# Kernel optimization log

Hardware: AMD Instinct MI355X
Metric: run time of the kernel (lower is better)

The kernel has to match this reference:

```python
import jax, jax.numpy as jnp
import numpy as np

N_SEG = 128      # number of ragged segments (boundaries has N_SEG+1 entries)
SEG_LEN = 128    # tokens per segment (regular boundaries)
D_IN = 1024      # input_size
H = 512          # hidden per direction; output_size = 2*H = 1024


def _run_dir(xs, W_ih, W_hh, b):
    """xs: [L, B, D] -> hidden states [L, B, H] for one direction.
    torch LSTM gate order: i, f, g, o."""
    xp = jnp.einsum('lbd,gd->lbg', xs, W_ih) + b  # precompute input projections [L,B,4H]
    B = xs.shape[1]
    Hh = W_hh.shape[1]

    def step(carry, gx):
        h, c = carry
        g = gx + h @ W_hh.T
        i, f, gg, o = jnp.split(g, 4, axis=-1)
        c = jax.nn.sigmoid(f) * c + jax.nn.sigmoid(i) * jnp.tanh(gg)
        h = jax.nn.sigmoid(o) * jnp.tanh(c)
        return (h, c), h

    z = jnp.zeros((B, Hh), xs.dtype)
    _, hs = jax.lax.scan(step, (z, z), xp)
    return hs


def _bilstm(x, W_ih_f, W_hh_f, b_f, W_ih_b, W_hh_b, b_b):
    hf = _run_dir(x, W_ih_f, W_hh_f, b_f)
    hb = _run_dir(x[::-1], W_ih_b, W_hh_b, b_b)[::-1]
    return jnp.concatenate([hf, hb], axis=-1)  # [L, B, 2H], fwd then bwd as in torch


def setup_inputs() -> dict:
    key = jax.random.key(0)
    ks = jax.random.split(key, 7)
    T = N_SEG * SEG_LEN
    s = 1.0 / np.sqrt(H)  # torch LSTM init scale
    u = lambda k, shape: jax.random.uniform(k, shape, jnp.float32, -s, s)
    return {
        'all_embs': jax.random.normal(ks[0], (T, D_IN), jnp.float32),
        'boundaries': jnp.arange(N_SEG + 1, dtype=jnp.int32) * SEG_LEN,
        'W_ih_f': u(ks[1], (4 * H, D_IN)),
        'W_hh_f': u(ks[2], (4 * H, H)),
        'b_f': u(ks[3], (4 * H,)),  # b_ih + b_hh folded together
        'W_ih_b': u(ks[4], (4 * H, D_IN)),
        'W_hh_b': u(ks[5], (4 * H, H)),
        'b_b': u(ks[6], (4 * H,)),
    }


def reference(all_embs, boundaries, W_ih_f, W_hh_f, b_f, W_ih_b, W_hh_b, b_b):
    n_seg = boundaries.shape[0] - 1
    T, D = all_embs.shape
    L = T // n_seg
    # regular boundaries: batch the per-segment LSTM calls into one scan
    x = all_embs.reshape(n_seg, L, D).transpose(1, 0, 2)  # [L, n_seg, D]
    y = _bilstm(x, W_ih_f, W_hh_f, b_f, W_ih_b, W_hh_b, b_b)  # [L, n_seg, 2H]
    out = y.transpose(1, 0, 2).reshape(T, 2 * H)
    # summarize=False: new boundaries equal old boundaries
    return (out, boundaries)
```

## Files before the change

### kernel.cpp

```cpp
#include <hip/hip_runtime.h>


typedef __attribute__((ext_vector_type(8))) short bf16x8;
typedef __attribute__((ext_vector_type(4))) float f32x4;

__device__ __forceinline__ unsigned short f2bf(float f) {
  unsigned int x = __builtin_bit_cast(unsigned int, f);
  x += 0x7fffu + ((x >> 16) & 1u);
  return (unsigned short)(x >> 16);
}
__device__ __forceinline__ float bf2f(unsigned short u) {
  unsigned int x = ((unsigned int)u) << 16;
  return __builtin_bit_cast(float, x);
}
__device__ __forceinline__ float sigm(float x) { return 1.f / (1.f + __expf(-x)); }
__device__ __forceinline__ float tanhfast(float x) {
  float e = __expf(2.f * x);
  return 1.f - 2.f / (e + 1.f);
}

__device__ __forceinline__ void gl_lds16(const void* g, void* l) {
  __builtin_amdgcn_global_load_lds((const __attribute__((address_space(1))) unsigned int*)g,
                                   (__attribute__((address_space(3))) unsigned int*)l, 16, 0, 0);
}
__device__ __forceinline__ void gl_lds16_llc(const void* g, void* l) {
  __builtin_amdgcn_global_load_lds((const __attribute__((address_space(1))) unsigned int*)g,
                                   (__attribute__((address_space(3))) unsigned int*)l, 16, 0, 17);
}

__global__ __launch_bounds__(256) void cast_x(const float* __restrict__ X,
                                              unsigned short* __restrict__ Xb) {
  const int i = blockIdx.x * 256 + threadIdx.x;
  const float4 v = ((const float4*)X)[i];
  uint2 o;
  o.x = (unsigned int)f2bf(v.x) | ((unsigned int)f2bf(v.y) << 16);
  o.y = (unsigned int)f2bf(v.z) | ((unsigned int)f2bf(v.w) << 16);
  ((uint2*)Xb)[i] = o;
}

__global__ __launch_bounds__(256) void pack_w(const float* __restrict__ Wif,
                                              const float* __restrict__ bf_,
                                              const float* __restrict__ Wib,
                                              const float* __restrict__ bb_,
                                              unsigned short* __restrict__ Wc,
                                              float* __restrict__ biasp) {
  const int pr = blockIdx.x;
  const int d = pr >> 11, r = pr & 2047;
  const float* src = (d ? Wib : Wif) + (size_t)r * 1024;
  const int t = threadIdx.x;
  const float4 v = ((const float4*)src)[t];
  uint2 o;
  o.x = (unsigned int)f2bf(v.x) | ((unsigned int)f2bf(v.y) << 16);
  o.y = (unsigned int)f2bf(v.z) | ((unsigned int)f2bf(v.w) << 16);
  ((uint2*)(Wc + (size_t)pr * 1024))[t] = o;
  if (t == 0) biasp[pr] = (d ? bb_ : bf_)[r];
}

__global__ __launch_bounds__(512) void gemm_xp(const unsigned short* __restrict__ A,
                                               const unsigned short* __restrict__ B,
                                               const float* __restrict__ bias,
                                               unsigned short* __restrict__ C) {
  __shared__ unsigned short SMEM[65536];
  const int tid = threadIdx.x;
  const int lane = tid & 63;
  const int wid = tid >> 6;
  const int wm = wid >> 2;
  const int wn = wid & 3;
  const int nid = blockIdx.x;
  const int xcd = nid & 7;
  const int ii = nid >> 3;
  const int bx = ii & 63;
  const int by = xcd * 2 + (ii >> 6);
  const long brow = (long)bx * 256;
  const long bcol = (long)by * 256;

  f32x4 acc[8][4];
  const f32x4 z = {0.f, 0.f, 0.f, 0.f};
#pragma unroll
  for (int m = 0; m < 8; ++m)
#pragma unroll
    for (int n = 0; n < 4; ++n) acc[m][n] = z;

  int srow[2], scol[2];
#pragma unroll
  for (int j = 0; j < 2; ++j) {
    const int o = (j * 512 + tid) * 16;
    srow[j] = o >> 7;
    scol[j] = (o & 127) ^ ((srow[j] & 7) << 4);
  }

#define STAGE_HALF(t, h, buf)                                                          \
  do {                                                                                 \
    const char* aA_ = (const char*)A + (brow + (h)*128) * 2048 + (t)*128;              \
    const char* aB_ = (const char*)B + (bcol + (h)*128) * 2048 + (t)*128;              \
    char* dA_ = (char*)(SMEM + ((buf)*2 + (h)) * 8192);                                \
    char* dB_ = (char*)(SMEM + 32768 + ((buf)*2 + (h)) * 8192);                        \
    _Pragma("unroll") for (int j_ = 0; j_ < 2; ++j_) {                                 \
      const int o_ = (j_ * 512 + tid) * 16;                                            \
      gl_lds16(aA_ + (long)srow[j_] * 2048 + scol[j_], dA_ + o_);                      \
      gl_lds16(aB_ + (long)srow[j_] * 2048 + scol[j_], dB_ + o_);                      \
    }                                                                                  \
  } while (0)

  STAGE_HALF(0, 0, 0);
  STAGE_HALF(0, 1, 0);

  const int p15 = lane & 15;
  const int kq = lane >> 4;

  for (int t = 0; t < 16; ++t) {
    const int cur = t & 1, nxt = cur ^ 1;
    const bool doStage = (t + 1 < 16);
    const unsigned short* Acur = SMEM + (cur * 2 + wm) * 8192;
    const unsigned short* Bcur = SMEM + 32768 + (cur * 2 + (wn >> 1)) * 8192;
#pragma unroll
    for (int p = 0; p < 4; ++p) {
      if (p < 2 && doStage) STAGE_HALF(t + 1, p, nxt);
      if (p == 0) {
        if (doStage)
          asm volatile("s_waitcnt vmcnt(4)" ::: "memory");
        else
          asm volatile("s_waitcnt vmcnt(0)" ::: "memory");
      }
      __builtin_amdgcn_s_barrier();
      bf16x8 af[2][2], bf[4][2];
#pragma unroll
      for (int mm = 0; mm < 2; ++mm) {
        const int ar = (2 * p + mm) * 16 + p15;
        const char* abase = (const char*)Acur + ar * 128;
        const int asw = (ar & 7) << 4;
#pragma unroll
        for (int kk = 0; kk < 2; ++kk)
          af[mm][kk] = *(const bf16x8*)(abase + ((kk * 64 + kq * 16) ^ asw));
      }
#pragma unroll
      for (int n = 0; n < 4; ++n) {
        const int br = (wn & 1) * 64 + n * 16 + p15;
        const char* bbase = (const char*)Bcur + br * 128;
        const int bsw = (br & 7) << 4;
#pragma unroll
        for (int kk = 0; kk < 2; ++kk)
          bf[n][kk] = *(const bf16x8*)(bbase + ((kk * 64 + kq * 16) ^ bsw));
      }
      __builtin_amdgcn_s_setprio(1);
#pragma unroll
      for (int kk = 0; kk < 2; ++kk)
#pragma unroll
        for (int mm = 0; mm < 2; ++mm)
#pragma unroll
          for (int n = 0; n < 4; ++n)
            acc[2 * p + mm][n] = __builtin_amdgcn_mfma_f32_16x16x32_bf16(
                af[mm][kk], bf[n][kk], acc[2 * p + mm][n], 0, 0, 0);
      __builtin_amdgcn_s_setprio(0);
      __builtin_amdgcn_s_barrier();
    }
  }
#undef STAGE_HALF

  __syncthreads();
  const int crow0 = wm * 128 + kq * 4;
  const int ccol0 = wn * 64 + p15;
#pragma unroll
  for (int m = 0; m < 8; ++m) {
#pragma unroll
    for (int n = 0; n < 4; ++n) {
      const int col = ccol0 + n * 16;
      const float bsv = bias[bcol + col];
#pragma unroll
      for (int r = 0; r < 4; ++r)
        SMEM[(crow0 + m * 16 + r) * 256 + col] = f2bf(acc[m][n][r] + bsv);
    }
  }
  __syncthreads();
#pragma unroll
  for (int i = 0; i < 16; ++i) {
    const int id = i * 512 + tid;
    const int row = id >> 5;
    const int c = id & 31;
    *(float4*)(C + (brow + row) * 4096 + bcol + c * 8) =
        *(const float4*)(SMEM + row * 256 + c * 8);
  }
}

__global__ __launch_bounds__(256, 1) void lstm_persist(
    const unsigned short* __restrict__ XPb, const float* __restrict__ Whf,
    const float* __restrict__ Whb, unsigned short* __restrict__ hb0,
    unsigned short* __restrict__ hb1, float* __restrict__ out,
    unsigned int* __restrict__ ctr) {
  __shared__ unsigned short A_s[8192];
  __shared__ unsigned short Hrep[16][32];

  const int tid = threadIdx.x;
  const int bid = blockIdx.x;
  const int ut = bid >> 4;
  const int grp = bid & 15;
  const int dir = grp >> 3;
  const int cs = grp & 7;
  const int lane = tid & 63;
  const int w = tid >> 6;
  const int p = lane & 15;
  const int kq8 = lane >> 4;
  const int hi = p >> 3;
  const int u_l = w * 8 + (p & 7);
  const int u_g = ut * 32 + u_l;
  unsigned int* const myctr = ctr + grp * 32;

  bf16x8 wreg[2][16];
  {
    const float* Wh = dir ? Whb : Whf;
#pragma unroll
    for (int f = 0; f < 2; ++f) {
      const int g = f * 2 + hi;
      const float* wrow = Wh + (size_t)(g * 512 + u_g) * 512 + kq8 * 8;
#pragma unroll
      for (int kk = 0; kk < 16; ++kk) {
        const float4 v0 = *(const float4*)(wrow + kk * 32);
        const float4 v1 = *(const float4*)(wrow + kk * 32 + 4);
        bf16x8 t;
        t[0] = (short)f2bf(v0.x); t[1] = (short)f2bf(v0.y);
        t[2] = (short)f2bf(v0.z); t[3] = (short)f2bf(v0.w);
        t[4] = (short)f2bf(v1.x); t[5] = (short)f2bf(v1.y);
        t[6] = (short)f2bf(v1.z); t[7] = (short)f2bf(v1.w);
        wreg[f][kk] = t;
      }
    }
  }

  float c_reg[2] = {0.f, 0.f};
  const size_t tileoff = (size_t)grp * 16384;
  const int cl0 = kq8 * 4 + 2 * hi;

  unsigned short xpr[2][4];
  {
    const int tcol0 = dir ? 127 : 0;
#pragma unroll
    for (int j = 0; j < 2; ++j) {
      const int seg = cs * 16 + cl0 + j;
      const size_t tok = (size_t)seg * 128 + tcol0;
      const unsigned short* xp = XPb + tok * 4096 + dir * 2048 + u_g;
#pragma unroll
      for (int g = 0; g < 4; ++g) xpr[j][g] = xp[g * 512];
    }
  }

  float phv[2];
  size_t pofs[2] = {0, 0};

  for (int tau = 0; tau < 128; ++tau) {
    const unsigned short* hc = (tau & 1) ? hb1 : hb0;
    unsigned short* hn = (tau & 1) ? hb0 : hb1;
    const int tcol = dir ? (127 - tau) : tau;

    {
      const char* srcb = (const char*)hc + tileoff;
      char* dstb = (char*)A_s;
#pragma unroll
      for (int j = 0; j < 4; ++j) {
        const int o = (j * 256 + tid) * 16;
        gl_lds16_llc(srcb + o, dstb + o);
      }
    }
    if (tau > 0) {
      out[pofs[0]] = phv[0];
      out[pofs[1]] = phv[1];
    }
    __syncthreads();

    unsigned short xprN[2][4];
    if (tau < 127) {
      const int tcolN = dir ? (126 - tau) : (tau + 1);
#pragma unroll
      for (int j = 0; j < 2; ++j) {
        const int seg = cs * 16 + cl0 + j;
        const size_t tok = (size_t)seg * 128 + tcolN;
        const unsigned short* xp = XPb + tok * 4096 + dir * 2048 + u_g;
#pragma unroll
        for (int g = 0; g < 4; ++g) xprN[j][g] = xp[g * 512];
      }
    }

    f32x4 accp[2][2];
    const f32x4 z = {0.f, 0.f, 0.f, 0.f};
    accp[0][0] = z; accp[0][1] = z; accp[1][0] = z; accp[1][1] = z;
    {
      const char* abase = (const char*)A_s + p * 1024;
      const int asw = (p & 7) << 4;
#pragma unroll
      for (int kk = 0; kk < 16; ++kk) {
        const int kb = kk * 64 + kq8 * 16;
        const bf16x8 af = *(const bf16x8*)(abase + (kb ^ asw));
        accp[0][kk & 1] =
            __builtin_amdgcn_mfma_f32_16x16x32_bf16(af, wreg[0][kk], accp[0][kk & 1], 0, 0, 0);
        accp[1][kk & 1] =
            __builtin_amdgcn_mfma_f32_16x16x32_bf16(af, wreg[1][kk], accp[1][kk & 1], 0, 0, 0);
      }
    }
    f32x4 acc0, acc1;
#pragma unroll
    for (int r = 0; r < 4; ++r) {
      acc0[r] = accp[0][0][r] + accp[0][1][r];
      acc1[r] = accp[1][0][r] + accp[1][1][r];
    }

    float hvr[2];
    {
      const float s0 = hi ? acc0[0] : acc0[2];
      const float s1 = hi ? acc0[1] : acc0[3];
      const float s2 = hi ? acc1[0] : acc1[2];
      const float s3 = hi ? acc1[1] : acc1[3];
      const float e0 = __shfl_xor(s0, 8);
      const float e1 = __shfl_xor(s1, 8);
      const float e2 = __shfl_xor(s2, 8);
      const float e3 = __shfl_xor(s3, 8);
      const float a0 = hi ? acc0[2] : acc0[0];
      const float a1 = hi ? acc0[3] : acc0[1];
      const float b0 = hi ? acc1[2] : acc1[0];
      const float b1 = hi ? acc1[3] : acc1[1];
      const float gi[2] = {hi ? e0 : a0, hi ? e1 : a1};
      const float gf[2] = {hi ? a0 : e0, hi ? a1 : e1};
      const float gg[2] = {hi ? e2 : b0, hi ? e3 : b1};
      const float go[2] = {hi ? b0 : e2, hi ? b1 : e3};
#pragma unroll
      for (int j = 0; j < 2; ++j) {
        const int cl = cl0 + j;
        const float pi = gi[j] + bf2f(xpr[j][0]);
        const float pf = gf[j] + bf2f(xpr[j][1]);
        const float pg = gg[j] + bf2f(xpr[j][2]);
        const float po = go[j] + bf2f(xpr[j][3]);
        float cv = sigm(pf) * c_reg[j] + sigm(pi) * tanhfast(pg);
        c_reg[j] = cv;
        hvr[j] = sigm(po) * tanhfast(cv);
        Hrep[cl][u_l] = f2bf(hvr[j]);
        const int seg = cs * 16 + cl;
        const size_t tok = (size_t)seg * 128 + tcol;
        pofs[j] = tok * 1024 + dir * 512 + u_g;
        phv[j] = hvr[j];
      }
    }
#pragma unroll
    for (int j = 0; j < 2; ++j)
#pragma unroll
      for (int g = 0; g < 4; ++g) xpr[j][g] = xprN[j][g];

    __syncthreads();

    if (tid < 128) {
      const int cl = tid >> 3, q = tid & 7;
      const unsigned long long v = *(const unsigned long long*)&Hrep[cl][q * 4];
      char* dst = (char*)hn + tileoff + cl * 1024 + ((ut * 64 + q * 8) ^ ((cl & 7) << 4));
      __hip_atomic_store((unsigned long long*)dst, v, __ATOMIC_RELAXED,
                         __HIP_MEMORY_SCOPE_AGENT);
    }

    __syncthreads();
    if (tid == 0) {
      const unsigned old =
          __hip_atomic_fetch_add(myctr, 1u, __ATOMIC_RELAXED, __HIP_MEMORY_SCOPE_AGENT);
      const unsigned tgt = (unsigned)(tau + 1) * 16u;
      if (old + 1u != tgt) {
        while (__hip_atomic_load(myctr, __ATOMIC_RELAXED, __HIP_MEMORY_SCOPE_AGENT) < tgt)
          __builtin_amdgcn_s_sleep(1);
      }
    }
    __syncthreads();
  }
  out[pofs[0]] = phv[0];
  out[pofs[1]] = phv[1];
}

__global__ void wr_bounds(const int* __restrict__ b, float* __restrict__ o) {
  const int i = threadIdx.x;
  if (i < 129) o[i] = (float)b[i];
}

extern "C" void kernel_launch(void* const* d_in, const int* in_sizes, int n_in,
                              void* d_out, int out_size, void* d_ws, size_t ws_size,
                              hipStream_t stream) {
  const float* X = (const float*)d_in[0];
  const int* bnd = (const int*)d_in[1];
  const float* Wif = (const float*)d_in[2];
  const float* Whf = (const float*)d_in[3];
  const float* bf_ = (const float*)d_in[4];
  const float* Wib = (const float*)d_in[5];
  const float* Whb = (const float*)d_in[6];
  const float* bb_ = (const float*)d_in[7];
  float* out = (float*)d_out;

  wr_bounds<<<1, 256, 0, stream>>>(bnd, out + 16777216);

  char* ws = (char*)d_ws;
  const size_t NEED = 176703488ULL;
  if (ws_size < NEED) return;

  unsigned short* XPb = (unsigned short*)(ws + 0);
  unsigned short* Xb = (unsigned short*)(ws + 134217728);
  unsigned short* Wc = (unsigned short*)(ws + 167772160);
  float* biasp = (float*)(ws + 176160768);
  unsigned short* hb0 = (unsigned short*)(ws + 176177152);
  unsigned short* hb1 = (unsigned short*)(ws + 176439296);
  unsigned int* ctrp = (unsigned int*)(ws + 176701440);

  cast_x<<<16384, 256, 0, stream>>>(X, Xb);
  pack_w<<<4096, 256, 0, stream>>>(Wif, bf_, Wib, bb_, Wc, biasp);
  gemm_xp<<<1024, 512, 0, stream>>>(Xb, Wc, biasp, XPb);

  hipMemsetAsync(hb0, 0, 262144, stream);
  hipMemsetAsync(ctrp, 0, 2048, stream);

  {
    const unsigned short* xpb = XPb;
    const float* whf = Whf;
    const float* whb = Whb;
    unsigned short* h0 = hb0;
    unsigned short* h1 = hb1;
    float* op = out;
    unsigned int* cp = ctrp;
    void* args[] = {&xpb, &whf, &whb, &h0, &h1, &op, &cp};
    hipError_t e = hipLaunchCooperativeKernel((const void*)lstm_persist, dim3(256), dim3(256),
                                              args, 0, stream);
    if (e != hipSuccess) {
      lstm_persist<<<256, 256, 0, stream>>>(XPb, Whf, Whb, hb0, hb1, out, ctrp);
    }
  }
}
```

Before: 491.8 us.

## Fuse input-projection GEMM with persistent BiLSTM via per-timestep readiness flags

Merges the input-projection GEMM and the persistent recurrent kernel into one cooperative launch. 128 blocks compute GEMM tiles in time-step order, alternating from both ends so forward and backward directions get their inputs early, and publish per-timestep-pair flags. The other 128 blocks run the recurrence with 512 threads (64 hidden units each, half as many blocks per sync group) and spin on those flags before loading each step's projections. The XP layout becomes time-major so each GEMM tile covers whole timesteps. The aim is to overlap the large GEMM with the latency-bound recurrence, at the cost of halving the recurrence block count, which adds per-step work and may slow the critical path while GEMM blocks compete for bandwidth.

```diff
diff --git a/kernel.cpp b/kernel.cpp
--- a/kernel.cpp
+++ b/kernel.cpp
@@ -56,316 +56,338 @@
   if (t == 0) biasp[pr] = (d ? bb_ : bf_)[r];
 }
 
-__global__ __launch_bounds__(512) void gemm_xp(const unsigned short* __restrict__ A,
-                                               const unsigned short* __restrict__ B,
-                                               const float* __restrict__ bias,
-                                               unsigned short* __restrict__ C) {
+__global__ __launch_bounds__(512, 1) void fused_bilstm(
+    const unsigned short* __restrict__ A,
+    const unsigned short* __restrict__ B,
+    const float* __restrict__ bias,
+    unsigned short* __restrict__ XPb,
+    const float* __restrict__ Whf, const float* __restrict__ Whb,
+    unsigned short* __restrict__ hb0, unsigned short* __restrict__ hb1,
+    float* __restrict__ out, unsigned int* __restrict__ ctr,
+    unsigned int* __restrict__ flags) {
   __shared__ unsigned short SMEM[65536];
   const int tid = threadIdx.x;
+  const int bidg = blockIdx.x;
   const int lane = tid & 63;
-  const int wid = tid >> 6;
-  const int wm = wid >> 2;
-  const int wn = wid & 3;
-  const int nid = blockIdx.x;
-  const int xcd = nid & 7;
-  const int ii = nid >> 3;
-  const int bx = ii & 63;
-  const int by = xcd * 2 + (ii >> 6);
-  const long brow = (long)bx * 256;
-  const long bcol = (long)by * 256;
-
-  f32x4 acc[8][4];
-  const f32x4 z = {0.f, 0.f, 0.f, 0.f};
-#pragma unroll
-  for (int m = 0; m < 8; ++m)
-#pragma unroll
-    for (int n = 0; n < 4; ++n) acc[m][n] = z;
-
-  int srow[2], scol[2];
-#pragma unroll
-  for (int j = 0; j < 2; ++j) {
-    const int o = (j * 512 + tid) * 16;
-    srow[j] = o >> 7;
-    scol[j] = (o & 127) ^ ((srow[j] & 7) << 4);
-  }
-
-#define STAGE_HALF(t, h, buf)                                                          \
-  do {                                                                                 \
-    const char* aA_ = (const char*)A + (brow + (h)*128) * 2048 + (t)*128;              \
-    const char* aB_ = (const char*)B + (bcol + (h)*128) * 2048 + (t)*128;              \
-    char* dA_ = (char*)(SMEM + ((buf)*2 + (h)) * 8192);                                \
-    char* dB_ = (char*)(SMEM + 32768 + ((buf)*2 + (h)) * 8192);                        \
-    _Pragma("unroll") for (int j_ = 0; j_ < 2; ++j_) {                                 \
-      const int o_ = (j_ * 512 + tid) * 16;                                            \
-      gl_lds16(aA_ + (long)srow[j_] * 2048 + scol[j_], dA_ + o_);                      \
-      gl_lds16(aB_ + (long)srow[j_] * 2048 + scol[j_], dB_ + o_);                      \
-    }                                                                                  \
+
+  if (bidg < 128) {
+    const int pid = bidg;
+    const int wid = tid >> 6;
+    const int wm = wid >> 2;
+    const int wn = wid & 3;
+    const int p15 = lane & 15;
+    const int kq = lane >> 4;
+
+    int srow[2], scol[2];
+#pragma unroll
+    for (int j = 0; j < 2; ++j) {
+      const int o = (j * 512 + tid) * 16;
+      srow[j] = o >> 7;
+      scol[j] = (o & 127) ^ ((srow[j] & 7) << 4);
+    }
+
+    for (int it = 0; it < 8; ++it) {
+      const int L = pid + it * 128;
+      const int k = L >> 4;
+      const int nt = L & 15;
+      const int pm = (k & 1) ? (63 - (k >> 1)) : (k >> 1);
+      const long brow = (long)pm * 256;
+      const long bcol = (long)nt * 256;
+
+      f32x4 acc[8][4];
+      const f32x4 z = {0.f, 0.f, 0.f, 0.f};
+#pragma unroll
+      for (int m = 0; m < 8; ++m)
+#pragma unroll
+        for (int n = 0; n < 4; ++n) acc[m][n] = z;
+
+#define STAGE_HALF(t, h, buf)                                                        \
+  do {                                                                               \
+    char* dA_ = (char*)(SMEM + ((buf)*2 + (h)) * 8192);                              \
+    char* dB_ = (char*)(SMEM + 32768 + ((buf)*2 + (h)) * 8192);                      \
+    _Pragma("unroll") for (int j_ = 0; j_ < 2; ++j_) {                               \
+      const int o_ = (j_ * 512 + tid) * 16;                                          \
+      const int rA_ = (int)brow + (h)*128 + srow[j_];                                \
+      const long tokA_ = ((long)(rA_ & 127) << 7) + (rA_ >> 7);                      \
+      gl_lds16((const char*)A + tokA_ * 2048 + (t)*128 + scol[j_], dA_ + o_);        \
+      const long rB_ = bcol + (h)*128 + srow[j_];                                    \
+      gl_lds16((const char*)B + rB_ * 2048 + (t)*128 + scol[j_], dB_ + o_);          \
+    }                                                                                \
   } while (0)
 
-  STAGE_HALF(0, 0, 0);
-  STAGE_HALF(0, 1, 0);
-
-  const int p15 = lane & 15;
-  const int kq = lane >> 4;
-
-  for (int t = 0; t < 16; ++t) {
-    const int cur = t & 1, nxt = cur ^ 1;
-    const bool doStage = (t + 1 < 16);
-    const unsigned short* Acur = SMEM + (cur * 2 + wm) * 8192;
-    const unsigned short* Bcur = SMEM + 32768 + (cur * 2 + (wn >> 1)) * 8192;
-#pragma unroll
-    for (int p = 0; p < 4; ++p) {
-      if (p < 2 && doStage) STAGE_HALF(t + 1, p, nxt);
-      if (p == 0) {
-        if (doStage)
-          asm volatile("s_waitcnt vmcnt(4)" ::: "memory");
-        else
-          asm volatile("s_waitcnt vmcnt(0)" ::: "memory");
-      }
-      __builtin_amdgcn_s_barrier();
-      bf16x8 af[2][2], bf[4][2];
-#pragma unroll
-      for (int mm = 0; mm < 2; ++mm) {
-        const int ar = (2 * p + mm) * 16 + p15;
-        const char* abase = (const char*)Acur + ar * 128;
-        const int asw = (ar & 7) << 4;
-#pragma unroll
-        for (int kk = 0; kk < 2; ++kk)
-          af[mm][kk] = *(const bf16x8*)(abase + ((kk * 64 + kq * 16) ^ asw));
-      }
-#pragma unroll
-      for (int n = 0; n < 4; ++n) {
-        const int br = (wn & 1) * 64 + n * 16 + p15;
-        const char* bbase = (const char*)Bcur + br * 128;
-        const int bsw = (br & 7) << 4;
-#pragma unroll
-        for (int kk = 0; kk < 2; ++kk)
-          bf[n][kk] = *(const bf16x8*)(bbase + ((kk * 64 + kq * 16) ^ bsw));
-      }
-      __builtin_amdgcn_s_setprio(1);
-#pragma unroll
-      for (int kk = 0; kk < 2; ++kk)
-#pragma unroll
-        for (int mm = 0; mm < 2; ++mm)
-#pragma unroll
-          for (int n = 0; n < 4; ++n)
-            acc[2 * p + mm][n] = __builtin_amdgcn_mfma_f32_16x16x32_bf16(
-                af[mm][kk], bf[n][kk], acc[2 * p + mm][n], 0, 0, 0);
-      __builtin_amdgcn_s_setprio(0);
-      __builtin_amdgcn_s_barrier();
-    }
-  }
+      STAGE_HALF(0, 0, 0);
+      STAGE_HALF(0, 1, 0);
+
+      for (int t = 0; t < 16; ++t) {
+        const int cur = t & 1, nxt = cur ^ 1;
+        const bool doStage = (t + 1 < 16);
+        const unsigned short* Acur = SMEM + (cur * 2 + wm) * 8192;
+        const unsigned short* Bcur = SMEM + 32768 + (cur * 2 + (wn >> 1)) * 8192;
+#pragma unroll
+        for (int p = 0; p < 4; ++p) {
+          if (p < 2 && doStage) STAGE_HALF(t + 1, p, nxt);
+          if (p == 0) {
+            if (doStage)
+              asm volatile("s_waitcnt vmcnt(4)" ::: "memory");
+            else
+              asm volatile("s_waitcnt vmcnt(0)" ::: "memory");
+          }
+          __builtin_amdgcn_s_barrier();
+          bf16x8 af[2][2], bf[4][2];
+#pragma unroll
+          for (int mm = 0; mm < 2; ++mm) {
+            const int ar = (2 * p + mm) * 16 + p15;
+            const char* abase = (const char*)Acur + ar * 128;
+            const int asw = (ar & 7) << 4;
+#pragma unroll
+            for (int kk = 0; kk < 2; ++kk)
+              af[mm][kk] = *(const bf16x8*)(abase + ((kk * 64 + kq * 16) ^ asw));
+          }
+#pragma unroll
+          for (int n = 0; n < 4; ++n) {
+            const int br = (wn & 1) * 64 + n * 16 + p15;
+            const char* bbase = (const char*)Bcur + br * 128;
+            const int bsw = (br & 7) << 4;
+#pragma unroll
+            for (int kk = 0; kk < 2; ++kk)
+              bf[n][kk] = *(const bf16x8*)(bbase + ((kk * 64 + kq * 16) ^ bsw));
+          }
+          __builtin_amdgcn_s_setprio(1);
+#pragma unroll
+          for (int kk = 0; kk < 2; ++kk)
+#pragma unroll
+            for (int mm = 0; mm < 2; ++mm)
+#pragma unroll
+              for (int n = 0; n < 4; ++n)
+                acc[2 * p + mm][n] = __builtin_amdgcn_mfma_f32_16x16x32_bf16(
+                    af[mm][kk], bf[n][kk], acc[2 * p + mm][n], 0, 0, 0);
+          __builtin_amdgcn_s_setprio(0);
+          __builtin_amdgcn_s_barrier();
+        }
+      }
 #undef STAGE_HALF
 
-  __syncthreads();
-  const int crow0 = wm * 128 + kq * 4;
-  const int ccol0 = wn * 64 + p15;
-#pragma unroll
-  for (int m = 0; m < 8; ++m) {
-#pragma unroll
-    for (int n = 0; n < 4; ++n) {
-      const int col = ccol0 + n * 16;
-      const float bsv = bias[bcol + col];
-#pragma unroll
-      for (int r = 0; r < 4; ++r)
-        SMEM[(crow0 + m * 16 + r) * 256 + col] = f2bf(acc[m][n][r] + bsv);
-    }
-  }
-  __syncthreads();
-#pragma unroll
-  for (int i = 0; i < 16; ++i) {
-    const int id = i * 512 + tid;
-    const int row = id >> 5;
-    const int c = id & 31;
-    *(float4*)(C + (brow + row) * 4096 + bcol + c * 8) =
-        *(const float4*)(SMEM + row * 256 + c * 8);
-  }
-}
-
-__global__ __launch_bounds__(256, 1) void lstm_persist(
-    const unsigned short* __restrict__ XPb, const float* __restrict__ Whf,
-    const float* __restrict__ Whb, unsigned short* __restrict__ hb0,
-    unsigned short* __restrict__ hb1, float* __restrict__ out,
-    unsigned int* __restrict__ ctr) {
-  __shared__ unsigned short A_s[8192];
-  __shared__ unsigned short Hrep[16][32];
-
-  const int tid = threadIdx.x;
-  const int bid = blockIdx.x;
-  const int ut = bid >> 4;
-  const int grp = bid & 15;
-  const int dir = grp >> 3;
-  const int cs = grp & 7;
-  const int lane = tid & 63;
-  const int w = tid >> 6;
-  const int p = lane & 15;
-  const int kq8 = lane >> 4;
-  const int hi = p >> 3;
-  const int u_l = w * 8 + (p & 7);
-  const int u_g = ut * 32 + u_l;
-  unsigned int* const myctr = ctr + grp * 32;
-
-  bf16x8 wreg[2][16];
-  {
-    const float* Wh = dir ? Whb : Whf;
-#pragma unroll
-    for (int f = 0; f < 2; ++f) {
-      const int g = f * 2 + hi;
-      const float* wrow = Wh + (size_t)(g * 512 + u_g) * 512 + kq8 * 8;
-#pragma unroll
-      for (int kk = 0; kk < 16; ++kk) {
-        const float4 v0 = *(const float4*)(wrow + kk * 32);
-        const float4 v1 = *(const float4*)(wrow + kk * 32 + 4);
-        bf16x8 t;
-        t[0] = (short)f2bf(v0.x); t[1] = (short)f2bf(v0.y);
-        t[2] = (short)f2bf(v0.z); t[3] = (short)f2bf(v0.w);
-        t[4] = (short)f2bf(v1.x); t[5] = (short)f2bf(v1.y);
-        t[6] = (short)f2bf(v1.z); t[7] = (short)f2bf(v1.w);
-        wreg[f][kk] = t;
-      }
-    }
-  }
-
-  float c_reg[2] = {0.f, 0.f};
-  const size_t tileoff = (size_t)grp * 16384;
-  const int cl0 = kq8 * 4 + 2 * hi;
-
-  unsigned short xpr[2][4];
-  {
-    const int tcol0 = dir ? 127 : 0;
-#pragma unroll
-    for (int j = 0; j < 2; ++j) {
-      const int seg = cs * 16 + cl0 + j;
-      const size_t tok = (size_t)seg * 128 + tcol0;
-      const unsigned short* xp = XPb + tok * 4096 + dir * 2048 + u_g;
-#pragma unroll
-      for (int g = 0; g < 4; ++g) xpr[j][g] = xp[g * 512];
-    }
-  }
-
-  float phv[2];
-  size_t pofs[2] = {0, 0};
-
-  for (int tau = 0; tau < 128; ++tau) {
-    const unsigned short* hc = (tau & 1) ? hb1 : hb0;
-    unsigned short* hn = (tau & 1) ? hb0 : hb1;
-    const int tcol = dir ? (127 - tau) : tau;
-
+      __syncthreads();
+      const int crow0 = wm * 128 + kq * 4;
+      const int ccol0 = wn * 64 + p15;
+#pragma unroll
+      for (int m = 0; m < 8; ++m) {
+#pragma unroll
+        for (int n = 0; n < 4; ++n) {
+          const int col = ccol0 + n * 16;
+          const float bsv = bias[bcol + col];
+#pragma unroll
+          for (int r = 0; r < 4; ++r)
+            SMEM[(crow0 + m * 16 + r) * 256 + col] = f2bf(acc[m][n][r] + bsv);
+        }
+      }
+      __syncthreads();
+#pragma unroll
+      for (int i = 0; i < 16; ++i) {
+        const int id = i * 512 + tid;
+        const int row = id >> 5;
+        const int c = id & 31;
+        *(float4*)(XPb + (brow + row) * 4096 + bcol + c * 8) =
+            *(const float4*)(SMEM + row * 256 + c * 8);
+      }
+      __syncthreads();
+      if (tid == 0) {
+        __hip_atomic_fetch_add(flags + pm * 32, 1u, __ATOMIC_RELEASE,
+                               __HIP_MEMORY_SCOPE_AGENT);
+      }
+      __syncthreads();
+    }
+  } else {
+    unsigned short* A_s = SMEM;
+    unsigned short(*Hrep)[64] = (unsigned short(*)[64])(SMEM + 8192);
+
+    const int cid = bidg - 128;
+    const int ut = cid >> 4;
+    const int grp = cid & 15;
+    const int dir = grp >> 3;
+    const int cs = grp & 7;
+    const int w = tid >> 6;
+    const int p = lane & 15;
+    const int kq8 = lane >> 4;
+    const int hi = p >> 3;
+    const int u_l = w * 8 + (p & 7);
+    const int u_g = ut * 64 + u_l;
+    unsigned int* const myctr = ctr + grp * 32;
+
+    bf16x8 wreg[2][16];
     {
-      const char* srcb = (const char*)hc + tileoff;
-      char* dstb = (char*)A_s;
-#pragma unroll
-      for (int j = 0; j < 4; ++j) {
-        const int o = (j * 256 + tid) * 16;
-        gl_lds16_llc(srcb + o, dstb + o);
-      }
-    }
-    if (tau > 0) {
-      out[pofs[0]] = phv[0];
-      out[pofs[1]] = phv[1];
-    }
-    __syncthreads();
-
-    unsigned short xprN[2][4];
-    if (tau < 127) {
-      const int tcolN = dir ? (126 - tau) : (tau + 1);
+      const float* Wh = dir ? Whb : Whf;
+#pragma unroll
+      for (int f = 0; f < 2; ++f) {
+        const int g = f * 2 + hi;
+        const float* wrow = Wh + (size_t)(g * 512 + u_g) * 512 + kq8 * 8;
+#pragma unroll
+        for (int kk = 0; kk < 16; ++kk) {
+          const float4 v0 = *(const float4*)(wrow + kk * 32);
+          const float4 v1 = *(const float4*)(wrow + kk * 32 + 4);
+          bf16x8 t;
+          t[0] = (short)f2bf(v0.x); t[1] = (short)f2bf(v0.y);
+          t[2] = (short)f2bf(v0.z); t[3] = (short)f2bf(v0.w);
+          t[4] = (short)f2bf(v1.x); t[5] = (short)f2bf(v1.y);
+          t[6] = (short)f2bf(v1.z); t[7] = (short)f2bf(v1.w);
+          wreg[f][kk] = t;
+        }
+      }
+    }
+
+    float c_reg[2] = {0.f, 0.f};
+    const size_t tileoff = (size_t)grp * 16384;
+    const int cl0 = kq8 * 4 + 2 * hi;
+
+    unsigned short xpr[2][4];
+    {
+      const int tcol0 = dir ? 127 : 0;
+      if (tid == 0) {
+        while (__hip_atomic_load(flags + (tcol0 >> 1) * 32, __ATOMIC_RELAXED,
+                                 __HIP_MEMORY_SCOPE_AGENT) < 16u)
+          __builtin_amdgcn_s_sleep(1);
+      }
+      __syncthreads();
 #pragma unroll
       for (int j = 0; j < 2; ++j) {
         const int seg = cs * 16 + cl0 + j;
-        const size_t tok = (size_t)seg * 128 + tcolN;
-        const unsigned short* xp = XPb + tok * 4096 + dir * 2048 + u_g;
-#pragma unroll
-        for (int g = 0; g < 4; ++g) xprN[j][g] = xp[g * 512];
-      }
-    }
-
-    f32x4 accp[2][2];
-    const f32x4 z = {0.f, 0.f, 0.f, 0.f};
-    accp[0][0] = z; accp[0][1] = z; accp[1][0] = z; accp[1][1] = z;
-    {
-      const char* abase = (const char*)A_s + p * 1024;
-      const int asw = (p & 7) << 4;
-#pragma unroll
-      for (int kk = 0; kk < 16; ++kk) {
-        const int kb = kk * 64 + kq8 * 16;
-        const bf16x8 af = *(const bf16x8*)(abase + (kb ^ asw));
-        accp[0][kk & 1] =
-            __builtin_amdgcn_mfma_f32_16x16x32_bf16(af, wreg[0][kk], accp[0][kk & 1], 0, 0, 0);
-        accp[1][kk & 1] =
-            __builtin_amdgcn_mfma_f32_16x16x32_bf16(af, wreg[1][kk], accp[1][kk & 1], 0, 0, 0);
-      }
-    }
-    f32x4 acc0, acc1;
-#pragma unroll
-    for (int r = 0; r < 4; ++r) {
-      acc0[r] = accp[0][0][r] + accp[0][1][r];
-      acc1[r] = accp[1][0][r] + accp[1][1][r];
-    }
-
-    float hvr[2];
-    {
-      const float s0 = hi ? acc0[0] : acc0[2];
-      const float s1 = hi ? acc0[1] : acc0[3];
-      const float s2 = hi ? acc1[0] : acc1[2];
-      const float s3 = hi ? acc1[1] : acc1[3];
-      const float e0 = __shfl_xor(s0, 8);
-      const float e1 = __shfl_xor(s1, 8);
-      const float e2 = __shfl_xor(s2, 8);
-      const float e3 = __shfl_xor(s3, 8);
-      const float a0 = hi ? acc0[2] : acc0[0];
-      const float a1 = hi ? acc0[3] : acc0[1];
-      const float b0 = hi ? acc1[2] : acc1[0];
-      const float b1 = hi ? acc1[3] : acc1[1];
-      const float gi[2] = {hi ? e0 : a0, hi ? e1 : a1};
-      const float gf[2] = {hi ? a0 : e0, hi ? a1 : e1};
-      const float gg[2] = {hi ? e2 : b0, hi ? e3 : b1};
-      const float go[2] = {hi ? b0 : e2, hi ? b1 : e3};
-#pragma unroll
-      for (int j = 0; j < 2; ++j) {
-        const int cl = cl0 + j;
-        const float pi = gi[j] + bf2f(xpr[j][0]);
-        const float pf = gf[j] + bf2f(xpr[j][1]);
-        const float pg = gg[j] + bf2f(xpr[j][2]);
-        const float po = go[j] + bf2f(xpr[j][3]);
-        float cv = sigm(pf) * c_reg[j] + sigm(pi) * tanhfast(pg);
-        c_reg[j] = cv;
-        hvr[j] = sigm(po) * tanhfast(cv);
-        Hrep[cl][u_l] = f2bf(hvr[j]);
-        const int seg = cs * 16 + cl;
-        const size_t tok = (size_t)seg * 128 + tcol;
-        pofs[j] = tok * 1024 + dir * 512 + u_g;
-        phv[j] = hvr[j];
-      }
-    }
-#pragma unroll
-    for (int j = 0; j < 2; ++j)
-#pragma unroll
-      for (int g = 0; g < 4; ++g) xpr[j][g] = xprN[j][g];
-
-    __syncthreads();
-
-    if (tid < 128) {
-      const int cl = tid >> 3, q = tid & 7;
-      const unsigned long long v = *(const unsigned long long*)&Hrep[cl][q * 4];
-      char* dst = (char*)hn + tileoff + cl * 1024 + ((ut * 64 + q * 8) ^ ((cl & 7) << 4));
-      __hip_atomic_store((unsigned long long*)dst, v, __ATOMIC_RELAXED,
-                         __HIP_MEMORY_SCOPE_AGENT);
-    }
-
-    __syncthreads();
-    if (tid == 0) {
-      const unsigned old =
-          __hip_atomic_fetch_add(myctr, 1u, __ATOMIC_RELAXED, __HIP_MEMORY_SCOPE_AGENT);
-      const unsigned tgt = (unsigned)(tau + 1) * 16u;
-      if (old + 1u != tgt) {
-        while (__hip_atomic_load(myctr, __ATOMIC_RELAXED, __HIP_MEMORY_SCOPE_AGENT) < tgt)
+        const size_t tokp = (size_t)tcol0 * 128 + seg;
+        const unsigned short* xp = XPb + tokp * 4096 + dir * 2048 + u_g;
+#pragma unroll
+        for (int g = 0; g < 4; ++g) xpr[j][g] = xp[g * 512];
+      }
+    }
+
+    float phv[2];
+    size_t pofs[2] = {0, 0};
+
+    for (int tau = 0; tau < 128; ++tau) {
+      const unsigned short* hc = (tau & 1) ? hb1 : hb0;
+      unsigned short* hn = (tau & 1) ? hb0 : hb1;
+      const int tcol = dir ? (127 - tau) : tau;
+
+      {
+        const char* srcb = (const char*)hc + tileoff;
+        char* dstb = (char*)A_s;
+#pragma unroll
+        for (int j = 0; j < 2; ++j) {
+          const int o = (j * 512 + tid) * 16;
+          gl_lds16_llc(srcb + o, dstb + o);
+        }
+      }
+      if (tau > 0) {
+        out[pofs[0]] = phv[0];
+        out[pofs[1]] = phv[1];
+      }
+      if (tau < 127 && tid == 0) {
+        const int tcolN = dir ? (126 - tau) : (tau + 1);
+        while (__hip_atomic_load(flags + (tcolN >> 1) * 32, __ATOMIC_RELAXED,
+                                 __HIP_MEMORY_SCOPE_AGENT) < 16u)
           __builtin_amdgcn_s_sleep(1);
       }
-    }
-    __syncthreads();
+      __syncthreads();
+
+      unsigned short xprN[2][4];
+      if (tau < 127) {
+        const int tcolN = dir ? (126 - tau) : (tau + 1);
+#pragma unroll
+        for (int j = 0; j < 2; ++j) {
+          const int seg = cs * 16 + cl0 + j;
+          const size_t tokp = (size_t)tcolN * 128 + seg;
+          const unsigned short* xp = XPb + tokp * 4096 + dir * 2048 + u_g;
+#pragma unroll
+          for (int g = 0; g < 4; ++g) xprN[j][g] = xp[g * 512];
+        }
+      }
+
+      f32x4 accp[2][2];
+      const f32x4 z = {0.f, 0.f, 0.f, 0.f};
+      accp[0][0] = z; accp[0][1] = z; accp[1][0] = z; accp[1][1] = z;
+      {
+        const char* abase = (const char*)A_s + p * 1024;
+        const int asw = (p & 7) << 4;
+#pragma unroll
+        for (int kk = 0; kk < 16; ++kk) {
+          const int kb = kk * 64 + kq8 * 16;
+          const bf16x8 af = *(const bf16x8*)(abase + (kb ^ asw));
+          accp[0][kk & 1] =
+              __builtin_amdgcn_mfma_f32_16x16x32_bf16(af, wreg[0][kk], accp[0][kk & 1], 0, 0, 0);
+          accp[1][kk & 1] =
+              __builtin_amdgcn_mfma_f32_16x16x32_bf16(af, wreg[1][kk], accp[1][kk & 1], 0, 0, 0);
+        }
+      }
+      f32x4 acc0, acc1;
+#pragma unroll
+      for (int r = 0; r < 4; ++r) {
+        acc0[r] = accp[0][0][r] + accp[0][1][r];
+        acc1[r] = accp[1][0][r] + accp[1][1][r];
+      }
+
+      float hvr[2];
+      {
+        const float s0 = hi ? acc0[0] : acc0[2];
+        const float s1 = hi ? acc0[1] : acc0[3];
+        const float s2 = hi ? acc1[0] : acc1[2];
+        const float s3 = hi ? acc1[1] : acc1[3];
+        const float e0 = __shfl_xor(s0, 8);
+        const float e1 = __shfl_xor(s1, 8);
+        const float e2 = __shfl_xor(s2, 8);
+        const float e3 = __shfl_xor(s3, 8);
+        const float a0 = hi ? acc0[2] : acc0[0];
+        const float a1 = hi ? acc0[3] : acc0[1];
+        const float b0 = hi ? acc1[2] : acc1[0];
+        const float b1 = hi ? acc1[3] : acc1[1];
+        const float gi[2] = {hi ? e0 : a0, hi ? e1 : a1};
+        const float gf[2] = {hi ? a0 : e0, hi ? a1 : e1};
+        const float gg[2] = {hi ? e2 : b0, hi ? e3 : b1};
+        const float go[2] = {hi ? b0 : e2, hi ? b1 : e3};
+#pragma unroll
+        for (int j = 0; j < 2; ++j) {
+          const int cl = cl0 + j;
+          const float pi = gi[j] + bf2f(xpr[j][0]);
+          const float pf = gf[j] + bf2f(xpr[j][1]);
+          const float pg = gg[j] + bf2f(xpr[j][2]);
+          const float po = go[j] + bf2f(xpr[j][3]);
+          float cv = sigm(pf) * c_reg[j] + sigm(pi) * tanhfast(pg);
+          c_reg[j] = cv;
+          hvr[j] = sigm(po) * tanhfast(cv);
+          Hrep[cl][u_l] = f2bf(hvr[j]);
+          const int seg = cs * 16 + cl;
+          const size_t tok = (size_t)seg * 128 + tcol;
+          pofs[j] = tok * 1024 + dir * 512 + u_g;
+          phv[j] = hvr[j];
+        }
+      }
+#pragma unroll
+      for (int j = 0; j < 2; ++j)
+#pragma unroll
+        for (int g = 0; g < 4; ++g) xpr[j][g] = xprN[j][g];
+
+      __syncthreads();
+
+      if (tid < 256) {
+        const int cl = tid >> 4, q = tid & 15;
+        const unsigned long long v = *(const unsigned long long*)&Hrep[cl][q * 4];
+        char* dst = (char*)hn + tileoff + cl * 1024 + ((ut * 128 + q * 8) ^ ((cl & 7) << 4));
+        __hip_atomic_store((unsigned long long*)dst, v, __ATOMIC_RELAXED,
+                           __HIP_MEMORY_SCOPE_AGENT);
+      }
+
+      __syncthreads();
+      if (tid == 0) {
+        const unsigned old =
+            __hip_atomic_fetch_add(myctr, 1u, __ATOMIC_RELAXED, __HIP_MEMORY_SCOPE_AGENT);
+        const unsigned tgt = (unsigned)(tau + 1) * 8u;
+        if (old + 1u != tgt) {
+          while (__hip_atomic_load(myctr, __ATOMIC_RELAXED, __HIP_MEMORY_SCOPE_AGENT) < tgt)
+            __builtin_amdgcn_s_sleep(1);
+        }
+      }
+      __syncthreads();
+    }
+    out[pofs[0]] = phv[0];
+    out[pofs[1]] = phv[1];
   }
-  out[pofs[0]] = phv[0];
-  out[pofs[1]] = phv[1];
 }
 
 __global__ void wr_bounds(const int* __restrict__ b, float* __restrict__ o) {
@@ -389,7 +411,7 @@
   wr_bounds<<<1, 256, 0, stream>>>(bnd, out + 16777216);
 
   char* ws = (char*)d_ws;
-  const size_t NEED = 176703488ULL;
+  const size_t NEED = 176711680ULL;
   if (ws_size < NEED) return;
 
   unsigned short* XPb = (unsigned short*)(ws + 0);
@@ -399,27 +421,33 @@
   unsigned short* hb0 = (unsigned short*)(ws + 176177152);
   unsigned short* hb1 = (unsigned short*)(ws + 176439296);
   unsigned int* ctrp = (unsigned int*)(ws + 176701440);
+  unsigned int* flagp = (unsigned int*)(ws + 176703488);
 
   cast_x<<<16384, 256, 0, stream>>>(X, Xb);
   pack_w<<<4096, 256, 0, stream>>>(Wif, bf_, Wib, bb_, Wc, biasp);
-  gemm_xp<<<1024, 512, 0, stream>>>(Xb, Wc, biasp, XPb);
 
   hipMemsetAsync(hb0, 0, 262144, stream);
   hipMemsetAsync(ctrp, 0, 2048, stream);
+  hipMemsetAsync(flagp, 0, 8192, stream);
 
   {
-    const unsigned short* xpb = XPb;
+    const unsigned short* a = Xb;
+    const unsigned short* b = Wc;
+    const float* bp = biasp;
+    unsigned short* xpb = XPb;
     const float* whf = Whf;
     const float* whb = Whb;
     unsigned short* h0 = hb0;
     unsigned short* h1 = hb1;
     float* op = out;
     unsigned int* cp = ctrp;
-    void* args[] = {&xpb, &whf, &whb, &h0, &h1, &op, &cp};
-    hipError_t e = hipLaunchCooperativeKernel((const void*)lstm_persist, dim3(256), dim3(256),
+    unsigned int* fp = flagp;
+    void* args[] = {&a, &b, &bp, &xpb, &whf, &whb, &h0, &h1, &op, &cp, &fp};
+    hipError_t e = hipLaunchCooperativeKernel((const void*)fused_bilstm, dim3(256), dim3(512),
                                               args, 0, stream);
     if (e != hipSuccess) {
-      lstm_persist<<<256, 256, 0, stream>>>(XPb, Whf, Whb, hb0, hb1, out, ctrp);
+      fused_bilstm<<<256, 512, 0, stream>>>(Xb, Wc, biasp, XPb, Whf, Whb, hb0, hb1, out, ctrp,
+                                            flagp);
     }
   }
 }
```

New measurement: 535.5 us. 8.9% more time.
